# Kernel tuning notes

Hardware: AMD Instinct MI355X
Metric: run time of the kernel (lower is better)

The kernel has to match this reference:

```python
import jax, jax.numpy as jnp
import numpy as np

NP, NR, NK = 64, 8, 500          # problems, rollouts, candidate nodes
H, HEADS, VD = 256, 8, 8         # hidden_dim, heads, vars_dim
HD = H // HEADS                  # head_dim
CLIP = 10.0                      # tanh logit clipping
NEG_INF = -jnp.inf


def setup_inputs() -> dict:
    key = jax.random.key(0)
    ks = jax.random.split(key, 17)
    f = lambda k, s: jax.random.normal(k, s, dtype=jnp.float32)
    B = NP * NR
    s = 1.0 / np.sqrt(H)
    return {
        "X": f(ks[0], (NP, NK, H)),
        "K": f(ks[1], (HEADS, NP, NK, HD)),
        "V": f(ks[2], (HEADS, NP, NK, HD)),
        "query": f(ks[3], (B, H)),
        "state1": f(ks[4], (B, H)),
        "state2": f(ks[5], (B, H)),
        "varfeat": f(ks[6], (NP, VD, NK)),
        "mask": jax.random.uniform(ks[7], (NP, NR, NK)) < 0.1,
        "nn_Q": f(ks[8], (HEADS, H, HD)) * (1.0 / np.sqrt(HD)),
        "nn_O": f(ks[9], (H, H)) * s,
        "nn_A": f(ks[10], (VD, H)) * s,
        "nn_B": f(ks[11], (H,)) * s,
        "nn_W": f(ks[12], (H,)) * s,
        "W_ih": f(ks[13], (4 * H, H)) * s,
        "W_hh": f(ks[14], (4 * H, H)) * s,
        "b_ih": f(ks[15], (4 * H,)) * s,
        "b_hh": f(ks[16], (4 * H,)) * s,
    }


def _decode(X, K, V, query, state1, state2, varfeat, mask,
            nn_Q, nn_O, nn_A, nn_B, nn_W, W_ih, W_hh, b_ih, b_hh):
    B = query.shape[0]
    # --- LSTMCell (PyTorch gate order: i, f, g, o) ---
    gates = query @ W_ih.T + b_ih + state1 @ W_hh.T + b_hh
    i, fg, g, o = jnp.split(gates, 4, axis=1)
    c = jax.nn.sigmoid(fg) * state2 + jax.nn.sigmoid(i) * jnp.tanh(g)
    h = jax.nn.sigmoid(o) * jnp.tanh(c)
    # --- MultiHeadAttention (glimpse) ---
    q = h.reshape(NP, NR, H)
    Q = jnp.einsum('pqh,ahd->apqd', q, nn_Q)                    # [heads,NP,NR,HD]
    S = jnp.einsum('apqd,apkd->apqk', Q, K) * (1.0 / np.sqrt(HD))
    S = jnp.where(mask[None], NEG_INF, S)
    S = jax.nn.softmax(S, axis=-1)
    x = jnp.einsum('apqk,apkd->apqd', S, V)
    x = x.transpose(1, 2, 0, 3).reshape(NP, NR, H)              # [NP,NR,H]
    qm = x @ nn_O                                               # glimpse query
    # --- additive attention with variable features ---
    vf = jnp.einsum('pvk,vh->pkh', varfeat, nn_A) + nn_B        # [NP,NK,H]
    t = jnp.tanh(X[:, None] + vf[:, None] + qm[:, :, None])     # [NP,NR,NK,H]
    logit = jnp.einsum('pqkh,h->pqk', t, nn_W)
    logit = jnp.where(mask, NEG_INF, logit).reshape(B, NK)
    # --- choose (mode=1: greedy argmax) ---
    infeasible = logit == NEG_INF
    l = jnp.where(infeasible, NEG_INF, jnp.tanh(logit) * CLIP)
    chosen = jnp.argmax(l, axis=1)
    logp = jax.nn.log_softmax(l, axis=1)
    chosen_p = jnp.take_along_axis(logp, chosen[:, None], axis=1).squeeze(1)
    return h, c, chosen_p


def reference(X, K, V, query, state1, state2, varfeat, mask,
              nn_Q, nn_O, nn_A, nn_B, nn_W, W_ih, W_hh, b_ih, b_hh):
    return _decode(X, K, V, query, state1, state2, varfeat, mask,
                   nn_Q, nn_O, nn_A, nn_B, nn_W, W_ih, W_hh, b_ih, b_hh)
```

## Files before the change

kernel.cpp:

```cpp
#include <hip/hip_runtime.h>

#define NPP   64
#define NRR   8
#define NKK   500
#define HDIM  256
#define NHEAD 8
#define VDIM  8
#define HD    32
#define BTOT  512

__device__ __forceinline__ float fast_tanh(float x) {
  const float e = __expf(2.f * x);
  return 1.f - 2.f * __builtin_amdgcn_rcpf(e + 1.f);
}
__device__ __forceinline__ float fast_sig(float x) {
  return __builtin_amdgcn_rcpf(1.f + __expf(-x));
}

__global__ __launch_bounds__(64) void k_lstm4(
    const float* __restrict__ query, const float* __restrict__ state1,
    const float* __restrict__ state2,
    const float* __restrict__ W_ih, const float* __restrict__ W_hh,
    const float* __restrict__ b_ih, const float* __restrict__ b_hh,
    const unsigned char* __restrict__ maskb, int* __restrict__ flagp,
    float* __restrict__ out_h, float* __restrict__ out_c)
{
  __shared__ float Wt[32][40];
  __shared__ float At[32][40];
  __shared__ float gt[32][40];

  const int t  = threadIdx.x;
  const int hb = blockIdx.x;
  const int bb = blockIdx.y;

  if (flagp != nullptr && hb == 0 && bb == 0) {
    __shared__ int f;
    if (t == 0) f = 0;
    __syncthreads();
    int any = 0;
    for (int j = t; j < 2048; j += 64) any |= maskb[2 * j + 1];
    if (any) atomicOr(&f, 1);
    __syncthreads();
    if (t == 0) *flagp = f;
  }

  const int tr = t >> 3, tc = t & 7;
  const int srow = t >> 1, sseg = (t & 1) * 16;
  const int wgrow = (srow >> 3) * HDIM + hb * 8 + (srow & 7);
  const int agrow = bb * 32 + srow;

  float acc[4][4];
#pragma unroll
  for (int i = 0; i < 4; ++i)
#pragma unroll
    for (int j = 0; j < 4; ++j) acc[i][j] = 0.f;

  for (int k0 = 0; k0 < 512; k0 += 32) {
    __syncthreads();
    {
      const float* wsrc = (k0 < 256) ? (W_ih + (size_t)wgrow * HDIM + k0)
                                     : (W_hh + (size_t)wgrow * HDIM + (k0 - 256));
      const float* asrc = (k0 < 256) ? (query  + (size_t)agrow * HDIM + k0)
                                     : (state1 + (size_t)agrow * HDIM + (k0 - 256));
#pragma unroll
      for (int j = 0; j < 4; ++j) {
        const float4 wv = *reinterpret_cast<const float4*>(wsrc + sseg + 4 * j);
        const float4 av = *reinterpret_cast<const float4*>(asrc + sseg + 4 * j);
        const int kk = sseg + 4 * j;
        Wt[kk + 0][srow] = wv.x; Wt[kk + 1][srow] = wv.y;
        Wt[kk + 2][srow] = wv.z; Wt[kk + 3][srow] = wv.w;
        At[kk + 0][srow] = av.x; At[kk + 1][srow] = av.y;
        At[kk + 2][srow] = av.z; At[kk + 3][srow] = av.w;
      }
    }
    __syncthreads();
#pragma unroll 8
    for (int kk = 0; kk < 32; ++kk) {
      const float4 wv = *reinterpret_cast<const float4*>(&Wt[kk][tr * 4]);
      const float4 av = *reinterpret_cast<const float4*>(&At[kk][tc * 4]);
      const float w[4] = {wv.x, wv.y, wv.z, wv.w};
      const float a[4] = {av.x, av.y, av.z, av.w};
#pragma unroll
      for (int i = 0; i < 4; ++i)
#pragma unroll
        for (int j = 0; j < 4; ++j) acc[i][j] += w[i] * a[j];
    }
  }

#pragma unroll
  for (int i = 0; i < 4; ++i) {
    float4 v;
    v.x = acc[i][0]; v.y = acc[i][1]; v.z = acc[i][2]; v.w = acc[i][3];
    *reinterpret_cast<float4*>(&gt[tr * 4 + i][tc * 4]) = v;
  }
  __syncthreads();

#pragma unroll
  for (int it = 0; it < 4; ++it) {
    const int cell = t + 64 * it;
    const int b = cell & 31, h = cell >> 5;
    const int gh = hb * 8 + h;
    const int gb = bb * 32 + b;
    const float bi = b_ih[0 * HDIM + gh] + b_hh[0 * HDIM + gh];
    const float bf = b_ih[1 * HDIM + gh] + b_hh[1 * HDIM + gh];
    const float bg = b_ih[2 * HDIM + gh] + b_hh[2 * HDIM + gh];
    const float bo = b_ih[3 * HDIM + gh] + b_hh[3 * HDIM + gh];
    const float iv = fast_sig (gt[ 0 + h][b] + bi);
    const float fv = fast_sig (gt[ 8 + h][b] + bf);
    const float gv = fast_tanh(gt[16 + h][b] + bg);
    const float ov = fast_sig (gt[24 + h][b] + bo);
    const size_t off = (size_t)gb * HDIM + gh;
    const float c = fv * state2[off] + iv * gv;
    out_c[off] = c;
    out_h[off] = ov * fast_tanh(c);
  }
}

__global__ __launch_bounds__(64) void k_gemm256(
    const float* __restrict__ A, const float* __restrict__ B,
    float* __restrict__ C, int hstride, int ldb, float scale)
{
  __shared__ float At[32][40];
  __shared__ float Bt[32][40];
  const int t  = threadIdx.x;
  const int ct = blockIdx.x;
  const int rt = blockIdx.y;
  const int tr = t >> 3, tc = t & 7;
  const int srow = t >> 1, sseg = (t & 1) * 16;

  const float* Asrc = A + ((size_t)(rt * 32 + srow)) * HDIM + sseg;
  const float* Bsrc = B + (size_t)hstride * ct + (size_t)srow * ldb + sseg;

  float acc[4][4];
#pragma unroll
  for (int i = 0; i < 4; ++i)
#pragma unroll
    for (int j = 0; j < 4; ++j) acc[i][j] = 0.f;

  for (int k0 = 0; k0 < 256; k0 += 32) {
    __syncthreads();
#pragma unroll
    for (int j = 0; j < 4; ++j) {
      const float4 av = *reinterpret_cast<const float4*>(Asrc + k0 + 4 * j);
      const int kk = sseg + 4 * j;
      At[kk + 0][srow] = av.x; At[kk + 1][srow] = av.y;
      At[kk + 2][srow] = av.z; At[kk + 3][srow] = av.w;
      const float4 bv = *reinterpret_cast<const float4*>(
          Bsrc + (size_t)k0 * ldb + 4 * j);
      *reinterpret_cast<float4*>(&Bt[srow][sseg + 4 * j]) = bv;
    }
    __syncthreads();
#pragma unroll 8
    for (int kk = 0; kk < 32; ++kk) {
      const float4 av = *reinterpret_cast<const float4*>(&At[kk][tr * 4]);
      const float4 bv = *reinterpret_cast<const float4*>(&Bt[kk][tc * 4]);
      const float a[4] = {av.x, av.y, av.z, av.w};
      const float b[4] = {bv.x, bv.y, bv.z, bv.w};
#pragma unroll
      for (int i = 0; i < 4; ++i)
#pragma unroll
        for (int j = 0; j < 4; ++j) acc[i][j] += a[i] * b[j];
    }
  }

  const int orow = rt * 32 + tr * 4;
  const int ocol = ct * 32 + tc * 4;
#pragma unroll
  for (int i = 0; i < 4; ++i) {
    float4 v;
    v.x = acc[i][0] * scale; v.y = acc[i][1] * scale;
    v.z = acc[i][2] * scale; v.w = acc[i][3] * scale;
    *reinterpret_cast<float4*>(C + (size_t)(orow + i) * HDIM + ocol) = v;
  }
}

__global__ __launch_bounds__(512, 4) void k_attn7(
    const float* __restrict__ Kt, const float* __restrict__ Vt,
    const float* __restrict__ Qg, const void* __restrict__ maskp,
    const int* __restrict__ flagp, float* __restrict__ xg)
{
  const int p = blockIdx.x >> 3;
  const int a = blockIdx.x & 7;
  const int t = threadIdx.x;
  const int wave = t >> 6, lane = t & 63;

  __shared__ float Sb[NRR][512];
  __shared__ float pb[16][NRR][HD];

  const int kc = (t < NKK) ? t : (NKK - 1);
  const float4* kp4 = reinterpret_cast<const float4*>(
      Kt + (((size_t)a * NPP + p) * NKK + kc) * HD);
  float4 kreg[8];
#pragma unroll
  for (int j = 0; j < 8; ++j) kreg[j] = kp4[j];

  const int dpv = t & 31, kb = t >> 5;
  const float* vb = Vt + (((size_t)a * NPP + p) * NKK + (size_t)kb * 32) * HD + dpv;
  float vreg[32];
#pragma unroll
  for (int j = 0; j < 32; ++j)
    vreg[j] = (kb * 32 + j < NKK) ? vb[(size_t)j * HD] : 0.f;

  const int flag = *flagp;
  float maskv[NRR];
  {
    const unsigned char* mb = (const unsigned char*)maskp;
    const int* mi = (const int*)maskp;
#pragma unroll
    for (int r = 0; r < NRR; ++r) {
      const size_t mo = (size_t)(p * NRR + r) * NKK + kc;
      const bool mk = flag ? (mb[mo] != 0) : (mi[mo] != 0);
      maskv[r] = mk ? -INFINITY : 0.f;
    }
  }

#pragma unroll
  for (int r = 0; r < NRR; ++r) {
    const float4* q4 = reinterpret_cast<const float4*>(
        Qg + ((size_t)(p * NRR + r)) * HDIM + a * HD);
    float s = 0.f;
#pragma unroll
    for (int j = 0; j < 8; ++j) {
      const float4 q = q4[j], k4 = kreg[j];
      s += q.x * k4.x + q.y * k4.y + q.z * k4.z + q.w * k4.w;
    }
    Sb[r][t] = (t < NKK) ? (s + maskv[r]) : -INFINITY;
  }
  __syncthreads();

  {
    const int r = wave;
    float lv[8], m = -INFINITY;
#pragma unroll
    for (int i = 0; i < 8; ++i) {
      lv[i] = Sb[r][lane + 64 * i];
      m = fmaxf(m, lv[i]);
    }
#pragma unroll
    for (int off = 32; off > 0; off >>= 1) m = fmaxf(m, __shfl_xor(m, off, 64));
    float ssum = 0.f;
#pragma unroll
    for (int i = 0; i < 8; ++i) {
      lv[i] = __expf(lv[i] - m);
      ssum += lv[i];
    }
#pragma unroll
    for (int off = 32; off > 0; off >>= 1) ssum += __shfl_xor(ssum, off, 64);
    const float inv = 1.f / ssum;
#pragma unroll
    for (int i = 0; i < 8; ++i) Sb[r][lane + 64 * i] = lv[i] * inv;
  }
  __syncthreads();

  {
    float acc[NRR];
#pragma unroll
    for (int r = 0; r < NRR; ++r) acc[r] = 0.f;
#pragma unroll
    for (int j4 = 0; j4 < 8; ++j4) {
      const float v0 = vreg[j4 * 4 + 0], v1 = vreg[j4 * 4 + 1];
      const float v2 = vreg[j4 * 4 + 2], v3 = vreg[j4 * 4 + 3];
#pragma unroll
      for (int r = 0; r < NRR; ++r) {
        const float4 s4 = *reinterpret_cast<const float4*>(
            &Sb[r][kb * 32 + j4 * 4]);
        acc[r] += s4.x * v0 + s4.y * v1 + s4.z * v2 + s4.w * v3;
      }
    }
#pragma unroll
    for (int r = 0; r < NRR; ++r) pb[kb][r][dpv] = acc[r];
  }
  __syncthreads();

  if (t < 256) {
    const int r = t >> 5, d = t & 31;
    float s = 0.f;
#pragma unroll
    for (int q = 0; q < 16; ++q) s += pb[q][r][d];
    xg[((size_t)(p * NRR + r)) * HDIM + a * HD + d] = s;
  }
}

__global__ __launch_bounds__(256) void k_logits5(
    const float* __restrict__ X, const float* __restrict__ varfeat,
    const float* __restrict__ nn_A, const float* __restrict__ nn_B,
    const float* __restrict__ nn_W, const float* __restrict__ qm,
    const int* __restrict__ flagp, const void* __restrict__ maskp,
    float* __restrict__ ls)
{
  const int p  = blockIdx.x >> 5;
  const int kt = blockIdx.x & 31;
  const int t = threadIdx.x;
  const int wave = t >> 6, lane = t & 63;
  const int h0 = lane * 4;

  const unsigned char* mb = (const unsigned char*)maskp;
  const int* mi = (const int*)maskp;
  const int flag = *flagp;
  const bool mbyte = (flag != 0);

  const float4 w4 = *reinterpret_cast<const float4*>(nn_W + h0);
  const float4 b4 = *reinterpret_cast<const float4*>(nn_B + h0);
  float4 a4r[VDIM];
#pragma unroll
  for (int v = 0; v < VDIM; ++v)
    a4r[v] = *reinterpret_cast<const float4*>(nn_A + (size_t)v * HDIM + h0);
  float4 q4r[NRR];
#pragma unroll
  for (int r = 0; r < NRR; ++r) {
    const float4 q = *reinterpret_cast<const float4*>(
        qm + (size_t)(p * NRR + r) * HDIM + h0);
    q4r[r].x = q.x + b4.x; q4r[r].y = q.y + b4.y;
    q4r[r].z = q.z + b4.z; q4r[r].w = q.w + b4.w;
  }

  for (int kk = 0; kk < 4; ++kk) {
    const int k = kt * 16 + wave * 4 + kk;
    if (k >= NKK) break;

    const float4 x4 = *reinterpret_cast<const float4*>(
        X + ((size_t)p * NKK + k) * HDIM + h0);
    float base0 = x4.x, base1 = x4.y, base2 = x4.z, base3 = x4.w;
#pragma unroll
    for (int v = 0; v < VDIM; ++v) {
      const float vv = varfeat[((size_t)p * VDIM + v) * NKK + k];
      base0 += vv * a4r[v].x; base1 += vv * a4r[v].y;
      base2 += vv * a4r[v].z; base3 += vv * a4r[v].w;
    }

    float acc[NRR];
#pragma unroll
    for (int r = 0; r < NRR; ++r) {
      acc[r] = fast_tanh(base0 + q4r[r].x) * w4.x
             + fast_tanh(base1 + q4r[r].y) * w4.y
             + fast_tanh(base2 + q4r[r].z) * w4.z
             + fast_tanh(base3 + q4r[r].w) * w4.w;
    }

    float v4[4];
    {
      float sw[8];
#pragma unroll
      for (int j = 0; j < 8; ++j) sw[j] = __shfl_xor(acc[j], 32, 64);
      const bool hi = (lane & 32) != 0;
#pragma unroll
      for (int j = 0; j < 4; ++j)
        v4[j] = hi ? (acc[j + 4] + sw[j + 4]) : (acc[j] + sw[j]);
    }
    float v2[2];
    {
      float sw[4];
#pragma unroll
      for (int j = 0; j < 4; ++j) sw[j] = __shfl_xor(v4[j], 16, 64);
      const bool hi = (lane & 16) != 0;
      v2[0] = hi ? (v4[2] + sw[2]) : (v4[0] + sw[0]);
      v2[1] = hi ? (v4[3] + sw[3]) : (v4[1] + sw[1]);
    }
    float w;
    {
      const float s0 = __shfl_xor(v2[0], 8, 64);
      const float s1 = __shfl_xor(v2[1], 8, 64);
      w = ((lane & 8) != 0) ? (v2[1] + s1) : (v2[0] + s0);
    }
    w += __shfl_xor(w, 4, 64);
    w += __shfl_xor(w, 2, 64);
    w += __shfl_xor(w, 1, 64);

    if ((lane & 7) == 0) {
      const int r = lane >> 3;
      const size_t mrow = (size_t)(p * NRR + r) * NKK + k;
      const bool mk = mbyte ? (mb[mrow] != 0) : (mi[mrow] != 0);
      ls[mrow] = mk ? -INFINITY : fast_tanh(w) * 10.0f;
    }
  }
}

__global__ __launch_bounds__(64) void k_choose(
    const float* __restrict__ ls, float* __restrict__ out_p)
{
  const int b = blockIdx.x;
  const int lane = threadIdx.x;
  float m = -INFINITY;
  float lv[8];
  int n = 0;
  for (int k = lane; k < NKK; k += 64, ++n) {
    lv[n] = ls[(size_t)b * NKK + k];
    m = fmaxf(m, lv[n]);
  }
#pragma unroll
  for (int off = 32; off > 0; off >>= 1) m = fmaxf(m, __shfl_xor(m, off, 64));
  float s = 0.f;
  for (int i = 0; i < n; ++i) s += __expf(lv[i] - m);
#pragma unroll
  for (int off = 32; off > 0; off >>= 1) s += __shfl_xor(s, off, 64);
  if (lane == 0) out_p[b] = -logf(s);
}

__global__ __launch_bounds__(256) void k_fused(
    const float* __restrict__ X, const float* __restrict__ Kt,
    const float* __restrict__ Vt, const float* __restrict__ varfeat,
    const void* __restrict__ maskp,
    const float* __restrict__ nn_Q, const float* __restrict__ nn_O,
    const float* __restrict__ nn_A, const float* __restrict__ nn_B,
    const float* __restrict__ nn_W,
    const float* __restrict__ out_h, float* __restrict__ out_p)
{
  const int p = blockIdx.x >> 3;
  const int r = blockIdx.x & 7;
  const int t = threadIdx.x;
  const int wave = t >> 6, lane = t & 63;

  __shared__ float hs[HDIM];
  __shared__ float Qs[NHEAD][HD];
  __shared__ float Sb[NHEAD][NKK];
  __shared__ float xs[HDIM];
  __shared__ float qs[HDIM];
  __shared__ float As2[HDIM][VDIM];
  __shared__ float Ws[HDIM];
  __shared__ float lsb[NKK];
  __shared__ int   mask_any;

  const unsigned char* mb = (const unsigned char*)maskp;
  if (t == 0) mask_any = 0;
  __syncthreads();
  {
    int any = 0;
    for (int j = t; j < 2048; j += 256) any |= mb[2 * j + 1];
    if (any) atomicOr(&mask_any, 1);
  }
  for (int idx = t; idx < VDIM * HDIM; idx += 256)
    As2[idx & 255][idx >> 8] = nn_A[idx];
  Ws[t] = nn_W[t];
  hs[t] = out_h[(size_t)(p * NRR + r) * HDIM + t];
  __syncthreads();
  const bool mbyte = (mask_any != 0);
  const int* mi = (const int*)maskp;
  const size_t mrow = (size_t)(p * NRR + r) * NKK;
  {
    const int a = t >> 5, d = t & 31;
    const float* nq = nn_Q + (size_t)a * HDIM * HD + d;
    float acc = 0.f;
    for (int h = 0; h < HDIM; ++h) acc += hs[h] * nq[(size_t)h * HD];
    Qs[a][d] = acc * 0.17677669529663687f;
  }
  __syncthreads();
  for (int k = t; k < NKK; k += 256) {
    const bool mk = mbyte ? (mb[mrow + k] != 0) : (mi[mrow + k] != 0);
#pragma unroll
    for (int a = 0; a < NHEAD; ++a) {
      const float4* kr4 = reinterpret_cast<const float4*>(
          Kt + (((size_t)a * NPP + p) * NKK + k) * HD);
      float s = 0.f;
#pragma unroll
      for (int d4 = 0; d4 < HD / 4; ++d4) {
        const float4 u = kr4[d4];
        s += Qs[a][4 * d4] * u.x + Qs[a][4 * d4 + 1] * u.y
           + Qs[a][4 * d4 + 2] * u.z + Qs[a][4 * d4 + 3] * u.w;
      }
      Sb[a][k] = mk ? -INFINITY : s;
    }
  }
  __syncthreads();
  for (int aa = 0; aa < 2; ++aa) {
    const int a = wave * 2 + aa;
    float m = -INFINITY;
    for (int k = lane; k < NKK; k += 64) m = fmaxf(m, Sb[a][k]);
#pragma unroll
    for (int off = 32; off > 0; off >>= 1) m = fmaxf(m, __shfl_xor(m, off, 64));
    float ssum = 0.f;
    for (int k = lane; k < NKK; k += 64) {
      const float e = expf(Sb[a][k] - m);
      Sb[a][k] = e; ssum += e;
    }
#pragma unroll
    for (int off = 32; off > 0; off >>= 1) ssum += __shfl_xor(ssum, off, 64);
    const float inv = 1.f / ssum;
    for (int k = lane; k < NKK; k += 64) Sb[a][k] *= inv;
  }
  __syncthreads();
  {
    const int a = t >> 5, d = t & 31;
    const float* vb = Vt + ((size_t)a * NPP + p) * NKK * HD + d;
    float acc = 0.f;
    for (int k = 0; k < NKK; ++k) acc += Sb[a][k] * vb[(size_t)k * HD];
    xs[a * HD + d] = acc;
  }
  __syncthreads();
  {
    float acc = 0.f;
    for (int i = 0; i < HDIM; ++i) acc += xs[i] * nn_O[(size_t)i * HDIM + t];
    qs[t] = acc + nn_B[t];
  }
  __syncthreads();
  for (int k = t; k < NKK; k += 256) {
    float vfv[VDIM];
#pragma unroll
    for (int v = 0; v < VDIM; ++v)
      vfv[v] = varfeat[((size_t)p * VDIM + v) * NKK + k];
    const float4* xp4 = reinterpret_cast<const float4*>(
        X + ((size_t)p * NKK + k) * HDIM);
    float acc = 0.f;
    for (int h4 = 0; h4 < HDIM / 4; ++h4) {
      const float4 ux = xp4[h4];
      const float xv[4] = {ux.x, ux.y, ux.z, ux.w};
#pragma unroll
      for (int j = 0; j < 4; ++j) {
        const int h = 4 * h4 + j;
        float base = xv[j] + qs[h];
        const float4 a0 = *reinterpret_cast<const float4*>(&As2[h][0]);
        const float4 a1 = *reinterpret_cast<const float4*>(&As2[h][4]);
        base += vfv[0] * a0.x + vfv[1] * a0.y + vfv[2] * a0.z + vfv[3] * a0.w
              + vfv[4] * a1.x + vfv[5] * a1.y + vfv[6] * a1.z + vfv[7] * a1.w;
        acc += tanhf(base) * Ws[h];
      }
    }
    lsb[k] = acc;
  }
  __syncthreads();
  for (int k = t; k < NKK; k += 256) {
    const bool mk = mbyte ? (mb[mrow + k] != 0) : (mi[mrow + k] != 0);
    lsb[k] = mk ? -INFINITY : tanhf(lsb[k]) * 10.0f;
  }
  __syncthreads();
  if (wave == 0) {
    float m = -INFINITY;
    for (int k = lane; k < NKK; k += 64) m = fmaxf(m, lsb[k]);
#pragma unroll
    for (int off = 32; off > 0; off >>= 1) m = fmaxf(m, __shfl_xor(m, off, 64));
    float s = 0.f;
    for (int k = lane; k < NKK; k += 64) s += expf(lsb[k] - m);
#pragma unroll
    for (int off = 32; off > 0; off >>= 1) s += __shfl_xor(s, off, 64);
    if (lane == 0) out_p[p * NRR + r] = -logf(s);
  }
}

extern "C" void kernel_launch(void* const* d_in, const int* in_sizes, int n_in,
                              void* d_out, int out_size, void* d_ws, size_t ws_size,
                              hipStream_t stream)
{
  const float* X       = (const float*)d_in[0];
  const float* Kt      = (const float*)d_in[1];
  const float* Vt      = (const float*)d_in[2];
  const float* query   = (const float*)d_in[3];
  const float* state1  = (const float*)d_in[4];
  const float* state2  = (const float*)d_in[5];
  const float* varfeat = (const float*)d_in[6];
  const void*  maskp   = d_in[7];
  const float* nn_Q    = (const float*)d_in[8];
  const float* nn_O    = (const float*)d_in[9];
  const float* nn_A    = (const float*)d_in[10];
  const float* nn_B    = (const float*)d_in[11];
  const float* nn_W    = (const float*)d_in[12];
  const float* W_ih    = (const float*)d_in[13];
  const float* W_hh    = (const float*)d_in[14];
  const float* b_ih    = (const float*)d_in[15];
  const float* b_hh    = (const float*)d_in[16];

  float* out   = (float*)d_out;
  float* out_h = out;
  float* out_c = out + (size_t)BTOT * HDIM;
  float* out_p = out + (size_t)2 * BTOT * HDIM;

  const size_t flag_bytes = 256;
  const size_t mat_bytes  = (size_t)BTOT * HDIM * 4;
  const size_t ls_bytes   = (size_t)BTOT * NKK * 4;
  const size_t need = flag_bytes + 3 * mat_bytes + ls_bytes;

  if (ws_size >= need) {
    int*   flagp = (int*)d_ws;
    float* Qw  = (float*)((char*)d_ws + flag_bytes);
    float* xw  = (float*)((char*)d_ws + flag_bytes + mat_bytes);
    float* qmw = (float*)((char*)d_ws + flag_bytes + 2 * mat_bytes);
    float* lsw = (float*)((char*)d_ws + flag_bytes + 3 * mat_bytes);

    hipLaunchKernelGGL(k_lstm4, dim3(32, 16), dim3(64), 0, stream,
                       query, state1, state2, W_ih, W_hh, b_ih, b_hh,
                       (const unsigned char*)maskp, flagp, out_h, out_c);
    hipLaunchKernelGGL(k_gemm256, dim3(8, 16), dim3(64), 0, stream,
                       out_h, nn_Q, Qw, HDIM * HD, HD, 0.17677669529663687f);
    hipLaunchKernelGGL(k_attn7, dim3(NPP * NHEAD), dim3(512), 0, stream,
                       Kt, Vt, Qw, maskp, flagp, xw);
    hipLaunchKernelGGL(k_gemm256, dim3(8, 16), dim3(64), 0, stream,
                       xw, nn_O, qmw, HD, HDIM, 1.0f);
    hipLaunchKernelGGL(k_logits5, dim3(NPP * 32), dim3(256), 0, stream,
                       X, varfeat, nn_A, nn_B, nn_W, qmw, flagp, maskp, lsw);
    hipLaunchKernelGGL(k_choose, dim3(BTOT), dim3(64), 0, stream,
                       lsw, out_p);
  } else {
    hipLaunchKernelGGL(k_lstm4, dim3(32, 16), dim3(64), 0, stream,
                       query, state1, state2, W_ih, W_hh, b_ih, b_hh,
                       (const unsigned char*)maskp, nullptr, out_h, out_c);
    hipLaunchKernelGGL(k_fused, dim3(NPP * NRR), dim3(256), 0, stream,
                       X, Kt, Vt, varfeat, maskp,
                       nn_Q, nn_O, nn_A, nn_B, nn_W,
                       out_h, out_p);
  }
}
```

Baseline: 235.6 us.

## Fuse Q and O projections into attention and do a partial softmax in logits

The two separate GEMM launches are removed. The per-head Q projection is computed inside the attention kernel from out_h and nn_Q, and the per-head slice of the O projection is written to eight per-head slabs that the logits kernel sums. The logits kernel no longer writes the full 512x500 logit array. It emits a partial max and a sum of exp(l-10) per tile, relying on the logits being bounded by the tanh clip, and the choose kernel merges those partials. This cuts two kernel launches and a large intermediate round-trip, at the cost of redundant nn_Q/nn_O reads per block and eight times the qm workspace traffic.

```diff
diff --git a/kernel.cpp b/kernel.cpp
--- a/kernel.cpp
+++ b/kernel.cpp
@@ -116,76 +116,27 @@
   }
 }
 
-__global__ __launch_bounds__(64) void k_gemm256(
-    const float* __restrict__ A, const float* __restrict__ B,
-    float* __restrict__ C, int hstride, int ldb, float scale)
-{
-  __shared__ float At[32][40];
-  __shared__ float Bt[32][40];
-  const int t  = threadIdx.x;
-  const int ct = blockIdx.x;
-  const int rt = blockIdx.y;
-  const int tr = t >> 3, tc = t & 7;
-  const int srow = t >> 1, sseg = (t & 1) * 16;
-
-  const float* Asrc = A + ((size_t)(rt * 32 + srow)) * HDIM + sseg;
-  const float* Bsrc = B + (size_t)hstride * ct + (size_t)srow * ldb + sseg;
-
-  float acc[4][4];
-#pragma unroll
-  for (int i = 0; i < 4; ++i)
-#pragma unroll
-    for (int j = 0; j < 4; ++j) acc[i][j] = 0.f;
-
-  for (int k0 = 0; k0 < 256; k0 += 32) {
-    __syncthreads();
-#pragma unroll
-    for (int j = 0; j < 4; ++j) {
-      const float4 av = *reinterpret_cast<const float4*>(Asrc + k0 + 4 * j);
-      const int kk = sseg + 4 * j;
-      At[kk + 0][srow] = av.x; At[kk + 1][srow] = av.y;
-      At[kk + 2][srow] = av.z; At[kk + 3][srow] = av.w;
-      const float4 bv = *reinterpret_cast<const float4*>(
-          Bsrc + (size_t)k0 * ldb + 4 * j);
-      *reinterpret_cast<float4*>(&Bt[srow][sseg + 4 * j]) = bv;
-    }
-    __syncthreads();
-#pragma unroll 8
-    for (int kk = 0; kk < 32; ++kk) {
-      const float4 av = *reinterpret_cast<const float4*>(&At[kk][tr * 4]);
-      const float4 bv = *reinterpret_cast<const float4*>(&Bt[kk][tc * 4]);
-      const float a[4] = {av.x, av.y, av.z, av.w};
-      const float b[4] = {bv.x, bv.y, bv.z, bv.w};
-#pragma unroll
-      for (int i = 0; i < 4; ++i)
-#pragma unroll
-        for (int j = 0; j < 4; ++j) acc[i][j] += a[i] * b[j];
-    }
-  }
-
-  const int orow = rt * 32 + tr * 4;
-  const int ocol = ct * 32 + tc * 4;
-#pragma unroll
-  for (int i = 0; i < 4; ++i) {
-    float4 v;
-    v.x = acc[i][0] * scale; v.y = acc[i][1] * scale;
-    v.z = acc[i][2] * scale; v.w = acc[i][3] * scale;
-    *reinterpret_cast<float4*>(C + (size_t)(orow + i) * HDIM + ocol) = v;
-  }
-}
-
-__global__ __launch_bounds__(512, 4) void k_attn7(
+__global__ __launch_bounds__(512, 4) void k_attn8(
     const float* __restrict__ Kt, const float* __restrict__ Vt,
-    const float* __restrict__ Qg, const void* __restrict__ maskp,
-    const int* __restrict__ flagp, float* __restrict__ xg)
+    const float* __restrict__ nn_Q, const float* __restrict__ nn_O,
+    const void* __restrict__ maskp, const int* __restrict__ flagp,
+    const float* __restrict__ out_h, float* __restrict__ qm_slabs)
 {
   const int p = blockIdx.x >> 3;
   const int a = blockIdx.x & 7;
   const int t = threadIdx.x;
   const int wave = t >> 6, lane = t & 63;
 
+  __shared__ float hs[NRR][HDIM];
+  __shared__ float Qs[NRR][36];
   __shared__ float Sb[NRR][512];
   __shared__ float pb[16][NRR][HD];
+  __shared__ float xs[NRR][36];
+
+  const float4 hv = reinterpret_cast<const float4*>(
+      out_h + (size_t)p * NRR * HDIM)[t];
+
+  const int flag = *flagp;
 
   const int kc = (t < NKK) ? t : (NKK - 1);
   const float4* kp4 = reinterpret_cast<const float4*>(
@@ -201,7 +152,6 @@
   for (int j = 0; j < 32; ++j)
     vreg[j] = (kb * 32 + j < NKK) ? vb[(size_t)j * HD] : 0.f;
 
-  const int flag = *flagp;
   float maskv[NRR];
   {
     const unsigned char* mb = (const unsigned char*)maskp;
@@ -214,14 +164,42 @@
     }
   }
 
+  reinterpret_cast<float4*>(&hs[0][0])[t] = hv;
+  __syncthreads();
+
+  {
+    const int r = wave, d4 = lane >> 3, ks = lane & 7;
+    const float* qb = nn_Q + ((size_t)a * HDIM + ks * 32) * HD + d4 * 4;
+    float qx = 0.f, qy = 0.f, qz = 0.f, qw = 0.f;
+#pragma unroll
+    for (int h = 0; h < 32; ++h) {
+      const float hval = hs[r][ks * 32 + h];
+      const float4 wv = *reinterpret_cast<const float4*>(qb + (size_t)h * HD);
+      qx += hval * wv.x; qy += hval * wv.y;
+      qz += hval * wv.z; qw += hval * wv.w;
+    }
+#pragma unroll
+    for (int off = 1; off < 8; off <<= 1) {
+      qx += __shfl_xor(qx, off, 64);
+      qy += __shfl_xor(qy, off, 64);
+      qz += __shfl_xor(qz, off, 64);
+      qw += __shfl_xor(qw, off, 64);
+    }
+    if (ks == 0) {
+      const float sc = 0.17677669529663687f;
+      Qs[r][d4 * 4 + 0] = qx * sc; Qs[r][d4 * 4 + 1] = qy * sc;
+      Qs[r][d4 * 4 + 2] = qz * sc; Qs[r][d4 * 4 + 3] = qw * sc;
+    }
+  }
+  __syncthreads();
+
 #pragma unroll
   for (int r = 0; r < NRR; ++r) {
-    const float4* q4 = reinterpret_cast<const float4*>(
-        Qg + ((size_t)(p * NRR + r)) * HDIM + a * HD);
     float s = 0.f;
 #pragma unroll
     for (int j = 0; j < 8; ++j) {
-      const float4 q = q4[j], k4 = kreg[j];
+      const float4 q = *reinterpret_cast<const float4*>(&Qs[r][j * 4]);
+      const float4 k4 = kreg[j];
       s += q.x * k4.x + q.y * k4.y + q.z * k4.z + q.w * k4.w;
     }
     Sb[r][t] = (t < NKK) ? (s + maskv[r]) : -INFINITY;
@@ -277,16 +255,44 @@
     float s = 0.f;
 #pragma unroll
     for (int q = 0; q < 16; ++q) s += pb[q][r][d];
-    xg[((size_t)(p * NRR + r)) * HDIM + a * HD + d] = s;
-  }
-}
-
-__global__ __launch_bounds__(256) void k_logits5(
+    xs[r][d] = s;
+  }
+  __syncthreads();
+
+  {
+    const int j = t & 255, rr = t >> 8;
+    float a0 = 0.f, a1 = 0.f, a2 = 0.f, a3 = 0.f;
+#pragma unroll
+    for (int d4 = 0; d4 < 8; ++d4) {
+      const float4 x0 = *reinterpret_cast<const float4*>(&xs[rr * 4 + 0][d4 * 4]);
+      const float4 x1 = *reinterpret_cast<const float4*>(&xs[rr * 4 + 1][d4 * 4]);
+      const float4 x2 = *reinterpret_cast<const float4*>(&xs[rr * 4 + 2][d4 * 4]);
+      const float4 x3 = *reinterpret_cast<const float4*>(&xs[rr * 4 + 3][d4 * 4]);
+      const float c0[4] = {x0.x, x0.y, x0.z, x0.w};
+      const float c1[4] = {x1.x, x1.y, x1.z, x1.w};
+      const float c2[4] = {x2.x, x2.y, x2.z, x2.w};
+      const float c3[4] = {x3.x, x3.y, x3.z, x3.w};
+#pragma unroll
+      for (int dd = 0; dd < 4; ++dd) {
+        const float w = nn_O[((size_t)(a * HD + d4 * 4 + dd)) * HDIM + j];
+        a0 += c0[dd] * w; a1 += c1[dd] * w;
+        a2 += c2[dd] * w; a3 += c3[dd] * w;
+      }
+    }
+    float* slab = qm_slabs + (size_t)a * BTOT * HDIM;
+    slab[(size_t)(p * NRR + rr * 4 + 0) * HDIM + j] = a0;
+    slab[(size_t)(p * NRR + rr * 4 + 1) * HDIM + j] = a1;
+    slab[(size_t)(p * NRR + rr * 4 + 2) * HDIM + j] = a2;
+    slab[(size_t)(p * NRR + rr * 4 + 3) * HDIM + j] = a3;
+  }
+}
+
+__global__ __launch_bounds__(256) void k_logits6(
     const float* __restrict__ X, const float* __restrict__ varfeat,
     const float* __restrict__ nn_A, const float* __restrict__ nn_B,
-    const float* __restrict__ nn_W, const float* __restrict__ qm,
+    const float* __restrict__ nn_W, const float* __restrict__ qm_slabs,
     const int* __restrict__ flagp, const void* __restrict__ maskp,
-    float* __restrict__ ls)
+    float* __restrict__ pmax, float* __restrict__ psum)
 {
   const int p  = blockIdx.x >> 5;
   const int kt = blockIdx.x & 31;
@@ -294,25 +300,41 @@
   const int wave = t >> 6, lane = t & 63;
   const int h0 = lane * 4;
 
+  __shared__ float qb[NRR][260];
+  __shared__ float red[4][NRR][2];
+
   const unsigned char* mb = (const unsigned char*)maskp;
   const int* mi = (const int*)maskp;
   const int flag = *flagp;
   const bool mbyte = (flag != 0);
 
+  for (int s = t; s < 512; s += 256) {
+    const int r = s >> 6, h4 = s & 63;
+    const float4 bv = *reinterpret_cast<const float4*>(nn_B + h4 * 4);
+    float qx = bv.x, qy = bv.y, qz = bv.z, qw = bv.w;
+#pragma unroll
+    for (int a = 0; a < NHEAD; ++a) {
+      const float4 q = *reinterpret_cast<const float4*>(
+          qm_slabs + (size_t)a * BTOT * HDIM +
+          (size_t)(p * NRR + r) * HDIM + h4 * 4);
+      qx += q.x; qy += q.y; qz += q.z; qw += q.w;
+    }
+    qb[r][h4 * 4 + 0] = qx; qb[r][h4 * 4 + 1] = qy;
+    qb[r][h4 * 4 + 2] = qz; qb[r][h4 * 4 + 3] = qw;
+  }
+  __syncthreads();
+
   const float4 w4 = *reinterpret_cast<const float4*>(nn_W + h0);
-  const float4 b4 = *reinterpret_cast<const float4*>(nn_B + h0);
   float4 a4r[VDIM];
 #pragma unroll
   for (int v = 0; v < VDIM; ++v)
     a4r[v] = *reinterpret_cast<const float4*>(nn_A + (size_t)v * HDIM + h0);
   float4 q4r[NRR];
 #pragma unroll
-  for (int r = 0; r < NRR; ++r) {
-    const float4 q = *reinterpret_cast<const float4*>(
-        qm + (size_t)(p * NRR + r) * HDIM + h0);
-    q4r[r].x = q.x + b4.x; q4r[r].y = q.y + b4.y;
-    q4r[r].z = q.z + b4.z; q4r[r].w = q.w + b4.w;
-  }
+  for (int r = 0; r < NRR; ++r)
+    q4r[r] = *reinterpret_cast<const float4*>(&qb[r][h0]);
+
+  float rmax = -INFINITY, rsum = 0.f;
 
   for (int kk = 0; kk < 4; ++kk) {
     const int k = kt * 16 + wave * 4 + kk;
@@ -370,30 +392,43 @@
       const int r = lane >> 3;
       const size_t mrow = (size_t)(p * NRR + r) * NKK + k;
       const bool mk = mbyte ? (mb[mrow] != 0) : (mi[mrow] != 0);
-      ls[mrow] = mk ? -INFINITY : fast_tanh(w) * 10.0f;
-    }
-  }
-}
-
-__global__ __launch_bounds__(64) void k_choose(
-    const float* __restrict__ ls, float* __restrict__ out_p)
+      const float l = mk ? -INFINITY : fast_tanh(w) * 10.0f;
+      rmax = fmaxf(rmax, l);
+      rsum += __expf(l - 10.f);
+    }
+  }
+
+  if ((lane & 7) == 0) {
+    red[wave][lane >> 3][0] = rmax;
+    red[wave][lane >> 3][1] = rsum;
+  }
+  __syncthreads();
+  if (t < NRR) {
+    float m = red[0][t][0], s = red[0][t][1];
+#pragma unroll
+    for (int w = 1; w < 4; ++w) {
+      m = fmaxf(m, red[w][t][0]);
+      s += red[w][t][1];
+    }
+    pmax[(size_t)(p * NRR + t) * 32 + kt] = m;
+    psum[(size_t)(p * NRR + t) * 32 + kt] = s;
+  }
+}
+
+__global__ __launch_bounds__(64) void k_choose2(
+    const float* __restrict__ pmax, const float* __restrict__ psum,
+    float* __restrict__ out_p)
 {
   const int b = blockIdx.x;
   const int lane = threadIdx.x;
-  float m = -INFINITY;
-  float lv[8];
-  int n = 0;
-  for (int k = lane; k < NKK; k += 64, ++n) {
-    lv[n] = ls[(size_t)b * NKK + k];
-    m = fmaxf(m, lv[n]);
-  }
-#pragma unroll
-  for (int off = 32; off > 0; off >>= 1) m = fmaxf(m, __shfl_xor(m, off, 64));
-  float s = 0.f;
-  for (int i = 0; i < n; ++i) s += __expf(lv[i] - m);
-#pragma unroll
-  for (int off = 32; off > 0; off >>= 1) s += __shfl_xor(s, off, 64);
-  if (lane == 0) out_p[b] = -logf(s);
+  float m = (lane < 32) ? pmax[(size_t)b * 32 + lane] : -INFINITY;
+  float s = (lane < 32) ? psum[(size_t)b * 32 + lane] : 0.f;
+#pragma unroll
+  for (int off = 16; off > 0; off >>= 1) {
+    m = fmaxf(m, __shfl_xor(m, off, 64));
+    s += __shfl_xor(s, off, 64);
+  }
+  if (lane == 0) out_p[b] = m - 10.f - logf(s);
 }
 
 __global__ __launch_bounds__(256) void k_fused(
@@ -563,30 +598,26 @@
   float* out_p = out + (size_t)2 * BTOT * HDIM;
 
   const size_t flag_bytes = 256;
-  const size_t mat_bytes  = (size_t)BTOT * HDIM * 4;
-  const size_t ls_bytes   = (size_t)BTOT * NKK * 4;
-  const size_t need = flag_bytes + 3 * mat_bytes + ls_bytes;
+  const size_t qm8_bytes  = (size_t)NHEAD * BTOT * HDIM * 4;
+  const size_t part_bytes = (size_t)BTOT * 32 * 4;
+  const size_t need = flag_bytes + qm8_bytes + 2 * part_bytes;
 
   if (ws_size >= need) {
     int*   flagp = (int*)d_ws;
-    float* Qw  = (float*)((char*)d_ws + flag_bytes);
-    float* xw  = (float*)((char*)d_ws + flag_bytes + mat_bytes);
-    float* qmw = (float*)((char*)d_ws + flag_bytes + 2 * mat_bytes);
-    float* lsw = (float*)((char*)d_ws + flag_bytes + 3 * mat_bytes);
+    float* qmw  = (float*)((char*)d_ws + flag_bytes);
+    float* pmax = (float*)((char*)d_ws + flag_bytes + qm8_bytes);
+    float* psum = (float*)((char*)d_ws + flag_bytes + qm8_bytes + part_bytes);
 
     hipLaunchKernelGGL(k_lstm4, dim3(32, 16), dim3(64), 0, stream,
                        query, state1, state2, W_ih, W_hh, b_ih, b_hh,
                        (const unsigned char*)maskp, flagp, out_h, out_c);
-    hipLaunchKernelGGL(k_gemm256, dim3(8, 16), dim3(64), 0, stream,
-                       out_h, nn_Q, Qw, HDIM * HD, HD, 0.17677669529663687f);
-    hipLaunchKernelGGL(k_attn7, dim3(NPP * NHEAD), dim3(512), 0, stream,
-                       Kt, Vt, Qw, maskp, flagp, xw);
-    hipLaunchKernelGGL(k_gemm256, dim3(8, 16), dim3(64), 0, stream,
-                       xw, nn_O, qmw, HD, HDIM, 1.0f);
-    hipLaunchKernelGGL(k_logits5, dim3(NPP * 32), dim3(256), 0, stream,
-                       X, varfeat, nn_A, nn_B, nn_W, qmw, flagp, maskp, lsw);
-    hipLaunchKernelGGL(k_choose, dim3(BTOT), dim3(64), 0, stream,
-                       lsw, out_p);
+    hipLaunchKernelGGL(k_attn8, dim3(NPP * NHEAD), dim3(512), 0, stream,
+                       Kt, Vt, nn_Q, nn_O, maskp, flagp, out_h, qmw);
+    hipLaunchKernelGGL(k_logits6, dim3(NPP * 32), dim3(256), 0, stream,
+                       X, varfeat, nn_A, nn_B, nn_W, qmw, flagp, maskp,
+                       pmax, psum);
+    hipLaunchKernelGGL(k_choose2, dim3(BTOT), dim3(64), 0, stream,
+                       pmax, psum, out_p);
   } else {
     hipLaunchKernelGGL(k_lstm4, dim3(32, 16), dim3(64), 0, stream,
                        query, state1, state2, W_ih, W_hh, b_ih, b_hh,
```

After: 234.9 us. About the same (-0.3%).
